# Kernel tuning notes

Hardware: AMD Instinct MI355X
Metric: run time of the kernel (lower is better)

Reference implementation:

```python
import jax, jax.numpy as jnp
import numpy as np

DIM = 2048          # args.dim
E = 16              # n_routed_experts
TOPK = 2            # n_activated_experts
H = 1408            # moe_inter_dim (expert hidden)
N_SHARED = 2        # n_shared_experts
HS = H * N_SHARED   # shared expert hidden
B, S = 2, 2048
TEMP = 1.0          # gate_temperature


def setup_inputs() -> dict:
    key = jax.random.key(0)
    ks = jax.random.split(key, 8)
    sc = 0.02
    return {
        "x": jax.random.normal(ks[0], (B, S, DIM), dtype=jnp.float32),
        "gate_w": jax.random.normal(ks[1], (E, DIM), dtype=jnp.float32) * sc,
        "w1": jax.random.normal(ks[2], (E, H, DIM), dtype=jnp.float32) * sc,
        "w2": jax.random.normal(ks[3], (E, DIM, H), dtype=jnp.float32) * sc,
        "w3": jax.random.normal(ks[4], (E, H, DIM), dtype=jnp.float32) * sc,
        "sw1": jax.random.normal(ks[5], (HS, DIM), dtype=jnp.float32) * sc,
        "sw2": jax.random.normal(ks[6], (DIM, HS), dtype=jnp.float32) * sc,
        "sw3": jax.random.normal(ks[7], (HS, DIM), dtype=jnp.float32) * sc,
    }


def reference(x, gate_w, w1, w2, w3, sw1, sw2, sw3):
    b, s, d = x.shape
    xf = x.reshape(-1, d)  # [T, D]

    # shared expert (SwiGLU FFN)
    sh = jax.nn.silu(xf @ sw1.T) * (xf @ sw3.T)      # [T, HS]
    shared_out = sh @ sw2.T                           # [T, D]

    # gate (eval mode: no input noise)
    scores = (xf @ gate_w.T) / TEMP                   # [T, E]
    probs = jax.nn.softmax(scores, axis=-1)
    topk_vals, topk_idx = jax.lax.top_k(probs, TOPK)  # sorted desc, matches torch.topk
    topk_vals = topk_vals / (topk_vals.sum(-1, keepdims=True) + 1e-9)

    # combine weights per (token, expert); zero where expert not selected
    w = (jax.nn.one_hot(topk_idx, E, dtype=xf.dtype) * topk_vals[..., None]).sum(1)  # [T, E]

    # all-expert SwiGLU, weighted-combined (w==0 exactly zeroes unselected experts)
    h1 = jnp.einsum('td,ehd->teh', xf, w1)            # [T, E, H]
    h3 = jnp.einsum('td,ehd->teh', xf, w3)
    act = jax.nn.silu(h1) * h3 * w[:, :, None]
    y = jnp.einsum('teh,edh->td', act, w2) + shared_out

    # aux load-balancing loss
    importance = probs.mean(0)                        # [E]
    load = w.sum(0) / (w.sum() + 1e-9)                # [E]
    aux_loss = E * (importance * load).sum()

    return y.reshape(b, s, d), aux_loss
```

## Files before the change

kernel.cpp:

```cpp
#include <hip/hip_runtime.h>
#include <cstdint>

#define TOKS 4096
#define DIMD 2048
#define NE   16
#define HE   1408
#define HSH  2816
#define SLOTS 8192
#define SLOTP 8320
#define MAXT 2048

typedef unsigned short u16;
typedef __attribute__((ext_vector_type(8))) __bf16 bf16x8;
typedef __attribute__((ext_vector_type(4))) float  f32x4;

__device__ inline unsigned f2bf_pack(float a, float b) {
  unsigned ua = __builtin_bit_cast(unsigned, a);
  unsigned ub = __builtin_bit_cast(unsigned, b);
  ua = (ua + 0x7FFFu + ((ua >> 16) & 1u)) >> 16;
  ub = (ub + 0x7FFFu + ((ub >> 16) & 1u)) >> 16;
  return ua | (ub << 16);
}
__device__ inline u16 f2bf(float a) {
  unsigned ua = __builtin_bit_cast(unsigned, a);
  return (u16)((ua + 0x7FFFu + ((ua >> 16) & 1u)) >> 16);
}
__device__ inline float bf2f(u16 u) {
  return __builtin_bit_cast(float, (unsigned)u << 16);
}
__device__ inline void gload_lds16(const u16* g, u16* l) {
  __builtin_amdgcn_global_load_lds((const __attribute__((address_space(1))) void*)g,
                                   (__attribute__((address_space(3))) void*)l, 16, 0, 0);
}

__global__ __launch_bounds__(64)
void gate2_kernel(const float* __restrict__ x, const float* __restrict__ gw,
                  float* __restrict__ probs, int* __restrict__ sel0, int* __restrict__ sel1,
                  float* __restrict__ wt0, float* __restrict__ wt1)
{
  const int t = blockIdx.x;
  const int l = threadIdx.x;
  const float4* xr = (const float4*)(x + (size_t)t * DIMD);
  float4 xv[8];
#pragma unroll
  for (int j = 0; j < 8; ++j) xv[j] = xr[j * 64 + l];

  float sc[16];
#pragma unroll
  for (int e = 0; e < 16; ++e) {
    const float4* g = (const float4*)(gw + (size_t)e * DIMD);
    float s = 0.f;
#pragma unroll
    for (int j = 0; j < 8; ++j) {
      float4 gv = g[j * 64 + l];
      s += xv[j].x * gv.x + xv[j].y * gv.y + xv[j].z * gv.z + xv[j].w * gv.w;
    }
#pragma unroll
    for (int o = 32; o > 0; o >>= 1) s += __shfl_down(s, o);
    sc[e] = s;
  }
  if (l == 0) {
    float mx = sc[0];
#pragma unroll
    for (int e = 1; e < 16; ++e) mx = fmaxf(mx, sc[e]);
    float pe[16]; float sum = 0.f;
#pragma unroll
    for (int e = 0; e < 16; ++e) { pe[e] = __expf(sc[e] - mx); sum += pe[e]; }
    float inv = 1.f / sum;
    int b0 = -1, b1 = -1; float v0 = -1.f, v1 = -1.f;
#pragma unroll
    for (int e = 0; e < 16; ++e) {
      float p = pe[e] * inv;
      probs[t * 16 + e] = p;
      if (p > v0) { v1 = v0; b1 = b0; v0 = p; b0 = e; }
      else if (p > v1) { v1 = p; b1 = e; }
    }
    float wsum = v0 + v1 + 1e-9f;
    sel0[t] = b0; sel1[t] = b1;
    wt0[t] = v0 / wsum; wt1[t] = v1 / wsum;
  }
}

__global__ __launch_bounds__(256)
void expert_count(const int* __restrict__ sel0, const int* __restrict__ sel1,
                  const float* __restrict__ wt0, const float* __restrict__ wt1,
                  int* __restrict__ counts, float* __restrict__ loadsum)
{
  const int e = blockIdx.x, tid = threadIdx.x;
  int c = 0; float s = 0.f;
  for (int t = tid; t < TOKS; t += 256) {
    if (sel0[t] == e) { c++; s += wt0[t]; }
    else if (sel1[t] == e) { c++; s += wt1[t]; }
  }
  __shared__ int ci[256]; __shared__ float sf[256];
  ci[tid] = c; sf[tid] = s; __syncthreads();
  for (int d = 128; d > 0; d >>= 1) {
    if (tid < d) { ci[tid] += ci[tid + d]; sf[tid] += sf[tid + d]; }
    __syncthreads();
  }
  if (tid == 0) { counts[e] = ci[0]; loadsum[e] = sf[0]; }
}

__global__ __launch_bounds__(256)
void offsets_aux(const float* __restrict__ probs, const int* __restrict__ counts,
                 const float* __restrict__ loadsum, int* __restrict__ offs,
                 int* __restrict__ te2, int* __restrict__ tn2, int* __restrict__ tm2,
                 int* __restrict__ me2,
                 int* __restrict__ te3, int* __restrict__ tn3, int* __restrict__ tm3,
                 int* __restrict__ me3,
                 float* __restrict__ out_aux)
{
  const int tid = threadIdx.x;
  float imp[16];
#pragma unroll
  for (int e = 0; e < 16; ++e) imp[e] = 0.f;
  for (int t = tid; t < TOKS; t += 256)
#pragma unroll
    for (int e = 0; e < 16; ++e) imp[e] += probs[t * 16 + e];

  __shared__ float red[256];
  __shared__ float impE[16];
  for (int e = 0; e < 16; ++e) {
    red[tid] = imp[e]; __syncthreads();
    for (int d = 128; d > 0; d >>= 1) {
      if (tid < d) red[tid] += red[tid + d];
      __syncthreads();
    }
    if (tid == 0) impE[e] = red[0];
    __syncthreads();
  }
  if (tid == 0) {
    int off = 0;
    for (int e = 0; e < 16; ++e) { offs[e] = off; off += counts[e]; }
    float tot = 0.f;
    for (int e = 0; e < 16; ++e) tot += loadsum[e];
    float aux = 0.f;
    for (int e = 0; e < 16; ++e) aux += (impE[e] / (float)TOKS) * (loadsum[e] / (tot + 1e-9f));
    *out_aux = 16.f * aux;
  }
  __syncthreads();
  if (tid < 16) {
    int e = tid;
    int mt_e = (counts[e] + 127) >> 7;
    {
      int base = 0;
      for (int ee = 0; ee < e; ++ee) base += ((counts[ee] + 127) >> 7) * 22;
      int idx = base;
      for (int n = 0; n < 22; ++n)
        for (int m = 0; m < mt_e; ++m) { te2[idx] = e; tn2[idx] = n; tm2[idx] = m << 7; ++idx; }
      if (e == 15) me2[0] = idx;
    }
    {
      int base = 0;
      for (int ee = 0; ee < e; ++ee) base += ((counts[ee] + 127) >> 7) * 16;
      int idx = base;
      for (int n = 0; n < 16; ++n)
        for (int m = 0; m < mt_e; ++m) { te3[idx] = e; tn3[idx] = n; tm3[idx] = m << 7; ++idx; }
      if (e == 15) me3[0] = idx;
    }
  }
}

__global__ __launch_bounds__(256)
void rank_scatter(const int* __restrict__ sel0, const int* __restrict__ sel1,
                  const float* __restrict__ wt0, const float* __restrict__ wt1,
                  const int* __restrict__ offs, int* __restrict__ toklist2,
                  float* __restrict__ slotwt, int* __restrict__ tokslot)
{
  const int e = blockIdx.x, tid = threadIdx.x;
  const int t0 = tid * 16;
  unsigned flags = 0; int cloc = 0;
#pragma unroll
  for (int j = 0; j < 16; ++j) {
    int t = t0 + j;
    bool f = (sel0[t] == e) || (sel1[t] == e);
    flags |= ((unsigned)f) << j;
    cloc += f;
  }
  __shared__ int psum[256];
  psum[tid] = cloc; __syncthreads();
  for (int d = 1; d < 256; d <<= 1) {
    int v = (tid >= d) ? psum[tid - d] : 0;
    __syncthreads();
    psum[tid] += v;
    __syncthreads();
  }
  int r = offs[e] + psum[tid] - cloc;
  for (int j = 0; j < 16; ++j) {
    if ((flags >> j) & 1u) {
      int t = t0 + j;
      bool first = (sel0[t] == e);
      toklist2[r] = t;
      slotwt[r] = first ? wt0[t] : wt1[t];
      tokslot[2 * t + (first ? 0 : 1)] = r;
      r++;
    }
  }
}

__global__ __launch_bounds__(256)
void cvt_f32_bf16(const float4* __restrict__ src, uint2* __restrict__ dst, int n4)
{
  int i = blockIdx.x * 256 + threadIdx.x;
  int stride = gridDim.x * 256;
  for (; i < n4; i += stride) {
    float4 v = src[i];
    uint2 p; p.x = f2bf_pack(v.x, v.y); p.y = f2bf_pack(v.z, v.w);
    dst[i] = p;
  }
}

__global__ __launch_bounds__(256)
void cvt_expert(const float4* __restrict__ src, uint2* __restrict__ dst,
                int per_e4, int dstride4, int doff4, int total4)
{
  int i = blockIdx.x * 256 + threadIdx.x;
  int stride = gridDim.x * 256;
  for (; i < total4; i += stride) {
    int e = i / per_e4;
    int r = i - e * per_e4;
    float4 v = src[i];
    uint2 p; p.x = f2bf_pack(v.x, v.y); p.y = f2bf_pack(v.z, v.w);
    dst[(size_t)e * dstride4 + doff4 + r] = p;
  }
}

__global__ __launch_bounds__(256)
void gather2(const float* __restrict__ x, const int* __restrict__ toklist2,
             u16* __restrict__ Xg)
{
  int slot = blockIdx.x * 4 + (threadIdx.x >> 6);
  int l = threadIdx.x & 63;
  int tok = toklist2[slot];
  const float4* srcr = (const float4*)(x + (size_t)tok * DIMD);
  uint2* dstr = (uint2*)(Xg + (size_t)slot * DIMD);
#pragma unroll
  for (int j = 0; j < 8; ++j) {
    float4 v = srcr[j * 64 + l];
    uint2 q; q.x = f2bf_pack(v.x, v.y); q.y = f2bf_pack(v.z, v.w);
    dstr[j * 64 + l] = q;
  }
}

template<int MODE>
__global__ __launch_bounds__(256, 3)
void gemm128(const u16* __restrict__ A, const u16* __restrict__ Bg,
             u16* __restrict__ Obf, float* __restrict__ Of,
             const int* __restrict__ counts, const int* __restrict__ offs,
             const int* __restrict__ te, const int* __restrict__ tn,
             const int* __restrict__ tm, const int* __restrict__ meta)
{
  constexpr int KD = (MODE == 0) ? DIMD : (MODE == 1) ? HSH : (MODE == 2) ? DIMD : HE;
  constexpr int ND = (MODE == 0) ? 2 * HSH : (MODE == 1) ? DIMD : (MODE == 2) ? HSH : DIMD;

  __shared__ u16 sA[128 * 64];
  __shared__ u16 sB[128 * 64];

  const int tid  = threadIdx.x;
  const int lane = tid & 63;
  const int wave = tid >> 6;
  const int wm = wave >> 1, wn = wave & 1;

  int mbase, nbase;
  int e = 0, cnt = 0, arow0;
  const u16* B = Bg;
  if constexpr (MODE >= 2) {
    int tix = blockIdx.x;
    if (tix >= meta[0]) return;
    e = te[tix];
    cnt = counts[e];
    mbase = tm[tix];
    nbase = tn[tix] * 128;
    arow0 = offs[e] + mbase;
    B = Bg + (size_t)e * ND * KD;
  } else {
    const int nx = gridDim.x;
    int bid = blockIdx.y * nx + blockIdx.x;
    int cpx = (nx * gridDim.y) >> 3;
    int swz = (bid & 7) * cpx + (bid >> 3);
    mbase = (swz / nx) * 128;
    nbase = (swz % nx) * 128;
    arow0 = mbase;
  }

  f32x4 acc[4][4];
#pragma unroll
  for (int i = 0; i < 4; ++i)
#pragma unroll
    for (int j = 0; j < 4; ++j) acc[i][j] = (f32x4){0.f, 0.f, 0.f, 0.f};

  const int srow  = lane >> 3;
  const int sslot = (lane & 7) ^ srow;
  const int scol  = sslot * 8;

  const u16* Bbase = B + (size_t)nbase * KD;

  for (int kb = 0; kb < KD; kb += 64) {
#pragma unroll
    for (int i = 0; i < 4; ++i) {
      int c = wave * 4 + i;
      int row = c * 8 + srow;
      size_t ar;
      if constexpr (MODE >= 2) {
        int rg = arow0 + row;
        if (rg > SLOTS - 1) rg = SLOTS - 1;
        ar = (size_t)rg * KD;
      } else {
        ar = (size_t)(arow0 + row) * KD;
      }
      gload_lds16(A + ar + kb + scol, &sA[c * 512]);
      gload_lds16(Bbase + (size_t)row * KD + kb + scol, &sB[c * 512]);
    }
    __syncthreads();

#pragma unroll
    for (int ks = 0; ks < 2; ++ks) {
      bf16x8 a[4], b[4];
#pragma unroll
      for (int mi = 0; mi < 4; ++mi) {
        int r = wm * 64 + mi * 16 + (lane & 15);
        int s = (ks * 4 + (lane >> 4)) ^ (r & 7);
        a[mi] = *(const bf16x8*)((const char*)sA + r * 128 + s * 16);
      }
#pragma unroll
      for (int ni = 0; ni < 4; ++ni) {
        int r = wn * 64 + ni * 16 + (lane & 15);
        int s = (ks * 4 + (lane >> 4)) ^ (r & 7);
        b[ni] = *(const bf16x8*)((const char*)sB + r * 128 + s * 16);
      }
#pragma unroll
      for (int mi = 0; mi < 4; ++mi)
#pragma unroll
        for (int ni = 0; ni < 4; ++ni)
          acc[mi][ni] = __builtin_amdgcn_mfma_f32_16x16x32_bf16(a[mi], b[ni], acc[mi][ni], 0, 0, 0);
    }
    __syncthreads();
  }

  const int lr4 = (lane >> 4) * 4;
  const int lc  = lane & 15;
#pragma unroll
  for (int mi = 0; mi < 4; ++mi) {
#pragma unroll
    for (int ni = 0; ni < 4; ++ni) {
#pragma unroll
      for (int r = 0; r < 4; ++r) {
        int lrow = wm * 64 + mi * 16 + lr4 + r;
        int col  = nbase + wn * 64 + ni * 16 + lc;
        float v = acc[mi][ni][r];
        if constexpr (MODE == 0) {
          Obf[(size_t)(mbase + lrow) * ND + col] = f2bf(v);
        } else if constexpr (MODE == 1) {
          Of[(size_t)(mbase + lrow) * ND + col] = v;
        } else {
          int grow = mbase + lrow;
          if (grow < cnt) Obf[(size_t)(arow0 + lrow) * ND + col] = f2bf(v);
        }
      }
    }
  }
}

__global__ __launch_bounds__(256)
void combine_sh(const u16* __restrict__ H, u16* __restrict__ U)
{
  int i = blockIdx.x * 256 + threadIdx.x;
  if (i >= TOKS * (HSH / 8)) return;
  int t = i / (HSH / 8);
  int c = (i - t * (HSH / 8)) * 8;
  const u16* h1p = H + (size_t)t * (2 * HSH) + c;
  uint4 va = *(const uint4*)h1p;
  uint4 vb = *(const uint4*)(h1p + HSH);
  const u16* ap = (const u16*)&va;
  const u16* bp = (const u16*)&vb;
  u16 o[8];
#pragma unroll
  for (int j = 0; j < 8; ++j) {
    float v1 = bf2f(ap[j]), v3 = bf2f(bp[j]);
    o[j] = f2bf((v1 / (1.f + __expf(-v1))) * v3);
  }
  *(uint4*)(U + (size_t)t * HSH + c) = *(const uint4*)o;
}

__global__ __launch_bounds__(256)
void combine_r(const u16* __restrict__ H, const float* __restrict__ slotwt,
               u16* __restrict__ Act)
{
  int i = blockIdx.x * 256 + threadIdx.x;
  if (i >= SLOTS * (HE / 8)) return;
  int t = i / (HE / 8);
  int c = (i - t * (HE / 8)) * 8;
  float wt = slotwt[t];
  const u16* h1p = H + (size_t)t * HSH + c;
  uint4 va = *(const uint4*)h1p;
  uint4 vb = *(const uint4*)(h1p + HE);
  const u16* ap = (const u16*)&va;
  const u16* bp = (const u16*)&vb;
  u16 o[8];
#pragma unroll
  for (int j = 0; j < 8; ++j) {
    float v1 = bf2f(ap[j]), v3 = bf2f(bp[j]);
    o[j] = f2bf((v1 / (1.f + __expf(-v1))) * v3 * wt);
  }
  *(uint4*)(Act + (size_t)t * HE + c) = *(const uint4*)o;
}

__global__ __launch_bounds__(256)
void finalize(const u16* __restrict__ Yslot, const int* __restrict__ tokslot,
              float* __restrict__ out)
{
  int i = blockIdx.x * 256 + threadIdx.x;
  int t = i >> 8;
  int c = (i & 255) * 8;
  int s0 = tokslot[2 * t], s1 = tokslot[2 * t + 1];
  uint4 a = *(const uint4*)(Yslot + (size_t)s0 * DIMD + c);
  uint4 b = *(const uint4*)(Yslot + (size_t)s1 * DIMD + c);
  const u16* ap = (const u16*)&a;
  const u16* bp = (const u16*)&b;
  float* op = out + (size_t)t * DIMD + c;
  float4 v0 = *(float4*)op, v1 = *(float4*)(op + 4);
  float vv[8] = {v0.x, v0.y, v0.z, v0.w, v1.x, v1.y, v1.z, v1.w};
#pragma unroll
  for (int j = 0; j < 8; ++j) vv[j] += bf2f(ap[j]) + bf2f(bp[j]);
  *(float4*)op = (float4){vv[0], vv[1], vv[2], vv[3]};
  *(float4*)(op + 4) = (float4){vv[4], vv[5], vv[6], vv[7]};
}

extern "C" void kernel_launch(void* const* d_in, const int* in_sizes, int n_in,
                              void* d_out, int out_size, void* d_ws, size_t ws_size,
                              hipStream_t stream) {
  const float* x      = (const float*)d_in[0];
  const float* gate_w = (const float*)d_in[1];
  const float* w1     = (const float*)d_in[2];
  const float* w2     = (const float*)d_in[3];
  const float* w3     = (const float*)d_in[4];
  const float* sw1    = (const float*)d_in[5];
  const float* sw2    = (const float*)d_in[6];
  const float* sw3    = (const float*)d_in[7];
  float* out = (float*)d_out;

  char* ws = (char*)d_ws;
  size_t o = 0;
  int*   counts   = (int*)(ws + o);   o += 256;
  int*   offsv    = (int*)(ws + o);   o += 256;
  float* loadsum  = (float*)(ws + o); o += 256;
  int*   te2      = (int*)(ws + o);   o += MAXT * 4;
  int*   tn2      = (int*)(ws + o);   o += MAXT * 4;
  int*   tm2      = (int*)(ws + o);   o += MAXT * 4;
  int*   me2      = (int*)(ws + o);   o += 256;
  int*   te3      = (int*)(ws + o);   o += MAXT * 4;
  int*   tn3      = (int*)(ws + o);   o += MAXT * 4;
  int*   tm3      = (int*)(ws + o);   o += MAXT * 4;
  int*   me3      = (int*)(ws + o);   o += 256;
  int*   sel0     = (int*)(ws + o);   o += TOKS * 4;
  int*   sel1     = (int*)(ws + o);   o += TOKS * 4;
  float* wt0      = (float*)(ws + o); o += TOKS * 4;
  float* wt1      = (float*)(ws + o); o += TOKS * 4;
  int*   tokslot  = (int*)(ws + o);   o += TOKS * 2 * 4;
  int*   toklist2 = (int*)(ws + o);   o += SLOTS * 4;
  float* slotwt   = (float*)(ws + o); o += SLOTS * 4;
  float* probs    = (float*)(ws + o); o += TOKS * 16 * 4;

  o = 1 << 20;
  u16* xbf   = (u16*)(ws + o); o += (size_t)TOKS * DIMD * 2;
  u16* Xg    = (u16*)(ws + o); o += (size_t)SLOTP * DIMD * 2;
  u16* w13b  = (u16*)(ws + o); o += (size_t)NE * HSH * DIMD * 2;
  u16* w2b   = (u16*)(ws + o); o += (size_t)NE * DIMD * HE * 2;
  u16* sw13b = (u16*)(ws + o); o += (size_t)(2 * HSH) * DIMD * 2;
  u16* sw2b  = (u16*)(ws + o); o += (size_t)DIMD * HSH * 2;
  u16* H     = (u16*)(ws + o); o += (size_t)SLOTP * HSH * 2;
  u16* UA    = (u16*)(ws + o); o += (size_t)SLOTP * HE * 2;
  u16* Yslot = Xg;

  gate2_kernel<<<TOKS, 64, 0, stream>>>(x, gate_w, probs, sel0, sel1, wt0, wt1);
  expert_count<<<NE, 256, 0, stream>>>(sel0, sel1, wt0, wt1, counts, loadsum);
  offsets_aux<<<1, 256, 0, stream>>>(probs, counts, loadsum, offsv,
                                     te2, tn2, tm2, me2, te3, tn3, tm3, me3,
                                     out + (size_t)TOKS * DIMD);
  rank_scatter<<<NE, 256, 0, stream>>>(sel0, sel1, wt0, wt1, offsv, toklist2, slotwt, tokslot);

  cvt_f32_bf16<<<2048, 256, 0, stream>>>((const float4*)x, (uint2*)xbf, TOKS * DIMD / 4);
  cvt_f32_bf16<<<1024, 256, 0, stream>>>((const float4*)sw1, (uint2*)sw13b, HSH * DIMD / 4);
  cvt_f32_bf16<<<1024, 256, 0, stream>>>((const float4*)sw3, (uint2*)sw13b + HSH * DIMD / 4, HSH * DIMD / 4);
  cvt_f32_bf16<<<1024, 256, 0, stream>>>((const float4*)sw2, (uint2*)sw2b, DIMD * HSH / 4);
  cvt_f32_bf16<<<4096, 256, 0, stream>>>((const float4*)w2, (uint2*)w2b, NE * DIMD * HE / 4);
  cvt_expert<<<4096, 256, 0, stream>>>((const float4*)w1, (uint2*)w13b,
                                       HE * DIMD / 4, HSH * DIMD / 4, 0, NE * HE * DIMD / 4);
  cvt_expert<<<4096, 256, 0, stream>>>((const float4*)w3, (uint2*)w13b,
                                       HE * DIMD / 4, HSH * DIMD / 4, HE * DIMD / 4, NE * HE * DIMD / 4);
  gather2<<<SLOTS / 4, 256, 0, stream>>>(x, toklist2, Xg);

  gemm128<0><<<dim3(2 * HSH / 128, TOKS / 128), 256, 0, stream>>>(
      xbf, sw13b, H, nullptr, nullptr, nullptr, nullptr, nullptr, nullptr, nullptr);
  combine_sh<<<TOKS * (HSH / 8) / 256, 256, 0, stream>>>(H, UA);
  gemm128<1><<<dim3(DIMD / 128, TOKS / 128), 256, 0, stream>>>(
      UA, sw2b, nullptr, out, nullptr, nullptr, nullptr, nullptr, nullptr, nullptr);

  gemm128<2><<<dim3(22 * 80), 256, 0, stream>>>(
      Xg, w13b, H, nullptr, counts, offsv, te2, tn2, tm2, me2);
  combine_r<<<SLOTS * (HE / 8) / 256, 256, 0, stream>>>(H, slotwt, UA);
  gemm128<3><<<dim3(16 * 80), 256, 0, stream>>>(
      UA, w2b, Yslot, nullptr, counts, offsv, te3, tn3, tm3, me3);
  finalize<<<TOKS * DIMD / 8 / 256, 256, 0, stream>>>(Yslot, tokslot, out);
}
```

Measured before the change: 790.4 us.

## Fuse SwiGLU combine into gate/up GEMM epilogue via interleaved w1/w3 layout

Weight conversion now interleaves w1 and w3 rows in blocks of 64, so each 128-wide N tile of the gate/up GEMM holds matching h1 and h3 columns. The epilogue exchanges the h3 half through shared memory and computes silu(h1)*h3, scaled by the slot weight for routed experts, before writing bf16. This removes the separate combine kernels and the round trip through the large intermediate H buffer. It also raises the occupancy hint to 4 blocks per SM and merges the w1/w3 conversion launches, at the cost of an extra barrier in the epilogue and half the waves idling while it runs.

```diff
diff --git a/kernel.cpp b/kernel.cpp
--- a/kernel.cpp
+++ b/kernel.cpp
@@ -211,17 +211,24 @@
 }
 
 __global__ __launch_bounds__(256)
-void cvt_expert(const float4* __restrict__ src, uint2* __restrict__ dst,
-                int per_e4, int dstride4, int doff4, int total4)
+void cvt_pair(const float4* __restrict__ src1, const float4* __restrict__ src3,
+              uint2* __restrict__ dst, int rows, int k4, int dstride4, int total4)
 {
   int i = blockIdx.x * 256 + threadIdx.x;
   int stride = gridDim.x * 256;
+  int per_e = rows * k4;
   for (; i < total4; i += stride) {
-    int e = i / per_e4;
-    int r = i - e * per_e4;
-    float4 v = src[i];
-    uint2 p; p.x = f2bf_pack(v.x, v.y); p.y = f2bf_pack(v.z, v.w);
-    dst[(size_t)e * dstride4 + doff4 + r] = p;
+    int e = i / per_e;
+    int rem = i - e * per_e;
+    int j = rem / k4;
+    int c = rem - j * k4;
+    size_t dbase = (size_t)e * dstride4 + (size_t)(((j >> 6) * 128 + (j & 63))) * k4 + c;
+    float4 v1 = src1[i];
+    uint2 p1; p1.x = f2bf_pack(v1.x, v1.y); p1.y = f2bf_pack(v1.z, v1.w);
+    dst[dbase] = p1;
+    float4 v3 = src3[i];
+    uint2 p3; p3.x = f2bf_pack(v3.x, v3.y); p3.y = f2bf_pack(v3.z, v3.w);
+    dst[dbase + (size_t)64 * k4] = p3;
   }
 }
 
@@ -243,18 +250,22 @@
 }
 
 template<int MODE>
-__global__ __launch_bounds__(256, 3)
+__global__ __launch_bounds__(256, 4)
 void gemm128(const u16* __restrict__ A, const u16* __restrict__ Bg,
              u16* __restrict__ Obf, float* __restrict__ Of,
              const int* __restrict__ counts, const int* __restrict__ offs,
              const int* __restrict__ te, const int* __restrict__ tn,
-             const int* __restrict__ tm, const int* __restrict__ meta)
+             const int* __restrict__ tm, const int* __restrict__ meta,
+             const float* __restrict__ slotwt)
 {
   constexpr int KD = (MODE == 0) ? DIMD : (MODE == 1) ? HSH : (MODE == 2) ? DIMD : HE;
   constexpr int ND = (MODE == 0) ? 2 * HSH : (MODE == 1) ? DIMD : (MODE == 2) ? HSH : DIMD;
-
-  __shared__ u16 sA[128 * 64];
-  __shared__ u16 sB[128 * 64];
+  constexpr bool FUSE = (MODE == 0 || MODE == 2);
+  constexpr int NDOUT = (MODE == 0) ? HSH : (MODE == 2) ? HE : ND;
+
+  __shared__ u16 sMem[2 * 128 * 64];
+  u16* sA = sMem;
+  u16* sB = sMem + 128 * 64;
 
   const int tid  = threadIdx.x;
   const int lane = tid & 63;
@@ -339,70 +350,64 @@
 
   const int lr4 = (lane >> 4) * 4;
   const int lc  = lane & 15;
-#pragma unroll
-  for (int mi = 0; mi < 4; ++mi) {
-#pragma unroll
-    for (int ni = 0; ni < 4; ++ni) {
-#pragma unroll
-      for (int r = 0; r < 4; ++r) {
-        int lrow = wm * 64 + mi * 16 + lr4 + r;
-        int col  = nbase + wn * 64 + ni * 16 + lc;
-        float v = acc[mi][ni][r];
-        if constexpr (MODE == 0) {
-          Obf[(size_t)(mbase + lrow) * ND + col] = f2bf(v);
-        } else if constexpr (MODE == 1) {
-          Of[(size_t)(mbase + lrow) * ND + col] = v;
-        } else {
-          int grow = mbase + lrow;
-          if (grow < cnt) Obf[(size_t)(arow0 + lrow) * ND + col] = f2bf(v);
+
+  if constexpr (FUSE) {
+    float* sX = (float*)sMem;
+    if (wn == 1) {
+#pragma unroll
+      for (int mi = 0; mi < 4; ++mi)
+#pragma unroll
+        for (int ni = 0; ni < 4; ++ni)
+#pragma unroll
+          for (int r = 0; r < 4; ++r)
+            sX[(wm * 64 + mi * 16 + lr4 + r) * 64 + ni * 16 + lc] = acc[mi][ni][r];
+    }
+    __syncthreads();
+    if (wn == 0) {
+#pragma unroll
+      for (int mi = 0; mi < 4; ++mi) {
+#pragma unroll
+        for (int ni = 0; ni < 4; ++ni) {
+#pragma unroll
+          for (int r = 0; r < 4; ++r) {
+            int lrow = wm * 64 + mi * 16 + lr4 + r;
+            float h1 = acc[mi][ni][r];
+            float h3 = sX[lrow * 64 + ni * 16 + lc];
+            float u = (h1 / (1.f + __expf(-h1))) * h3;
+            int col = (nbase >> 1) + ni * 16 + lc;
+            if constexpr (MODE == 0) {
+              Obf[(size_t)(mbase + lrow) * NDOUT + col] = f2bf(u);
+            } else {
+              int grow = mbase + lrow;
+              if (grow < cnt) {
+                u *= slotwt[arow0 + lrow];
+                Obf[(size_t)(arow0 + lrow) * NDOUT + col] = f2bf(u);
+              }
+            }
+          }
         }
       }
     }
-  }
-}
-
-__global__ __launch_bounds__(256)
-void combine_sh(const u16* __restrict__ H, u16* __restrict__ U)
-{
-  int i = blockIdx.x * 256 + threadIdx.x;
-  if (i >= TOKS * (HSH / 8)) return;
-  int t = i / (HSH / 8);
-  int c = (i - t * (HSH / 8)) * 8;
-  const u16* h1p = H + (size_t)t * (2 * HSH) + c;
-  uint4 va = *(const uint4*)h1p;
-  uint4 vb = *(const uint4*)(h1p + HSH);
-  const u16* ap = (const u16*)&va;
-  const u16* bp = (const u16*)&vb;
-  u16 o[8];
-#pragma unroll
-  for (int j = 0; j < 8; ++j) {
-    float v1 = bf2f(ap[j]), v3 = bf2f(bp[j]);
-    o[j] = f2bf((v1 / (1.f + __expf(-v1))) * v3);
-  }
-  *(uint4*)(U + (size_t)t * HSH + c) = *(const uint4*)o;
-}
-
-__global__ __launch_bounds__(256)
-void combine_r(const u16* __restrict__ H, const float* __restrict__ slotwt,
-               u16* __restrict__ Act)
-{
-  int i = blockIdx.x * 256 + threadIdx.x;
-  if (i >= SLOTS * (HE / 8)) return;
-  int t = i / (HE / 8);
-  int c = (i - t * (HE / 8)) * 8;
-  float wt = slotwt[t];
-  const u16* h1p = H + (size_t)t * HSH + c;
-  uint4 va = *(const uint4*)h1p;
-  uint4 vb = *(const uint4*)(h1p + HE);
-  const u16* ap = (const u16*)&va;
-  const u16* bp = (const u16*)&vb;
-  u16 o[8];
-#pragma unroll
-  for (int j = 0; j < 8; ++j) {
-    float v1 = bf2f(ap[j]), v3 = bf2f(bp[j]);
-    o[j] = f2bf((v1 / (1.f + __expf(-v1))) * v3 * wt);
-  }
-  *(uint4*)(Act + (size_t)t * HE + c) = *(const uint4*)o;
+  } else {
+#pragma unroll
+    for (int mi = 0; mi < 4; ++mi) {
+#pragma unroll
+      for (int ni = 0; ni < 4; ++ni) {
+#pragma unroll
+        for (int r = 0; r < 4; ++r) {
+          int lrow = wm * 64 + mi * 16 + lr4 + r;
+          int col  = nbase + wn * 64 + ni * 16 + lc;
+          float v = acc[mi][ni][r];
+          if constexpr (MODE == 1) {
+            Of[(size_t)(mbase + lrow) * ND + col] = v;
+          } else {
+            int grow = mbase + lrow;
+            if (grow < cnt) Obf[(size_t)(arow0 + lrow) * ND + col] = f2bf(v);
+          }
+        }
+      }
+    }
+  }
 }
 
 __global__ __launch_bounds__(256)
@@ -468,8 +473,7 @@
   u16* w2b   = (u16*)(ws + o); o += (size_t)NE * DIMD * HE * 2;
   u16* sw13b = (u16*)(ws + o); o += (size_t)(2 * HSH) * DIMD * 2;
   u16* sw2b  = (u16*)(ws + o); o += (size_t)DIMD * HSH * 2;
-  u16* H     = (u16*)(ws + o); o += (size_t)SLOTP * HSH * 2;
-  u16* UA    = (u16*)(ws + o); o += (size_t)SLOTP * HE * 2;
+  u16* UA    = (u16*)(ws + o); o += (size_t)SLOTP * HSH * 2;
   u16* Yslot = Xg;
 
   gate2_kernel<<<TOKS, 64, 0, stream>>>(x, gate_w, probs, sel0, sel1, wt0, wt1);
@@ -480,26 +484,22 @@
   rank_scatter<<<NE, 256, 0, stream>>>(sel0, sel1, wt0, wt1, offsv, toklist2, slotwt, tokslot);
 
   cvt_f32_bf16<<<2048, 256, 0, stream>>>((const float4*)x, (uint2*)xbf, TOKS * DIMD / 4);
-  cvt_f32_bf16<<<1024, 256, 0, stream>>>((const float4*)sw1, (uint2*)sw13b, HSH * DIMD / 4);
-  cvt_f32_bf16<<<1024, 256, 0, stream>>>((const float4*)sw3, (uint2*)sw13b + HSH * DIMD / 4, HSH * DIMD / 4);
+  cvt_pair<<<2048, 256, 0, stream>>>((const float4*)sw1, (const float4*)sw3, (uint2*)sw13b,
+                                     HSH, DIMD / 4, 0, HSH * DIMD / 4);
   cvt_f32_bf16<<<1024, 256, 0, stream>>>((const float4*)sw2, (uint2*)sw2b, DIMD * HSH / 4);
   cvt_f32_bf16<<<4096, 256, 0, stream>>>((const float4*)w2, (uint2*)w2b, NE * DIMD * HE / 4);
-  cvt_expert<<<4096, 256, 0, stream>>>((const float4*)w1, (uint2*)w13b,
-                                       HE * DIMD / 4, HSH * DIMD / 4, 0, NE * HE * DIMD / 4);
-  cvt_expert<<<4096, 256, 0, stream>>>((const float4*)w3, (uint2*)w13b,
-                                       HE * DIMD / 4, HSH * DIMD / 4, HE * DIMD / 4, NE * HE * DIMD / 4);
+  cvt_pair<<<4096, 256, 0, stream>>>((const float4*)w1, (const float4*)w3, (uint2*)w13b,
+                                     HE, DIMD / 4, HSH * DIMD / 4, NE * HE * DIMD / 4);
   gather2<<<SLOTS / 4, 256, 0, stream>>>(x, toklist2, Xg);
 
   gemm128<0><<<dim3(2 * HSH / 128, TOKS / 128), 256, 0, stream>>>(
-      xbf, sw13b, H, nullptr, nullptr, nullptr, nullptr, nullptr, nullptr, nullptr);
-  combine_sh<<<TOKS * (HSH / 8) / 256, 256, 0, stream>>>(H, UA);
+      xbf, sw13b, UA, nullptr, nullptr, nullptr, nullptr, nullptr, nullptr, nullptr, nullptr);
   gemm128<1><<<dim3(DIMD / 128, TOKS / 128), 256, 0, stream>>>(
-      UA, sw2b, nullptr, out, nullptr, nullptr, nullptr, nullptr, nullptr, nullptr);
+      UA, sw2b, nullptr, out, nullptr, nullptr, nullptr, nullptr, nullptr, nullptr, nullptr);
 
   gemm128<2><<<dim3(22 * 80), 256, 0, stream>>>(
-      Xg, w13b, H, nullptr, counts, offsv, te2, tn2, tm2, me2);
-  combine_r<<<SLOTS * (HE / 8) / 256, 256, 0, stream>>>(H, slotwt, UA);
+      Xg, w13b, UA, nullptr, counts, offsv, te2, tn2, tm2, me2, slotwt);
   gemm128<3><<<dim3(16 * 80), 256, 0, stream>>>(
-      UA, w2b, Yslot, nullptr, counts, offsv, te3, tn3, tm3, me3);
+      UA, w2b, Yslot, nullptr, counts, offsv, te3, tn3, tm3, me3, nullptr);
   finalize<<<TOKS * DIMD / 8 / 256, 256, 0, stream>>>(Yslot, tokslot, out);
 }
```

Result: no change. 776.3 us (-1.8%).
